# Kernel tuning notes

Measured on AMD Instinct MI355X. Metric: run time of the kernel, lower is better.

The kernel has to match this reference:

```python
import jax, jax.numpy as jnp
import numpy as np

EMBED_DIM = 512
N_HEADS = 8
HEAD_DIM = EMBED_DIM // N_HEADS


def setup_inputs() -> dict:
    key = jax.random.key(0)
    ks = jax.random.split(key, 8)
    B, S, D = 8, 2048, EMBED_DIM
    scale = 1.0 / np.sqrt(D)
    return {
        "key": jax.random.normal(ks[0], (B, S, D), dtype=jnp.float32),
        "query": jax.random.normal(ks[1], (B, S, D), dtype=jnp.float32),
        "value": jax.random.normal(ks[2], (B, S, D), dtype=jnp.float32),
        # nn.Linear stores weight as [out, in]; y = x @ W.T. We store W_T=[in,out].
        "Wq": jax.random.normal(ks[3], (D, D), dtype=jnp.float32) * scale,
        "Wk": jax.random.normal(ks[4], (D, D), dtype=jnp.float32) * scale,
        "Wv": jax.random.normal(ks[5], (D, D), dtype=jnp.float32) * scale,
        "Wo": jax.random.normal(ks[6], (D, D), dtype=jnp.float32) * scale,
        "bo": jax.random.normal(ks[7], (D,), dtype=jnp.float32) * scale,
    }


def reference(key, query, value, Wq, Wk, Wv, Wo, bo):
    B, S, D = key.shape
    Sq = query.shape[1]
    H, Hd = N_HEADS, HEAD_DIM
    # projections (no bias for q/k/v)
    q = (query @ Wq).reshape(B, Sq, H, Hd)
    k = (key @ Wk).reshape(B, S, H, Hd)
    v = (value @ Wv).reshape(B, S, H, Hd)
    # scores: [B, H, Sq, S]
    product = jnp.einsum("bqhd,bkhd->bhqk", q, k) / np.sqrt(Hd)
    scores = jax.nn.softmax(product, axis=-1)
    out = jnp.einsum("bhqk,bkhd->bqhd", scores, v).reshape(B, Sq, D)
    return out @ Wo + bo
```

## Files before the change

kernel.cpp:

```cpp
#include <hip/hip_runtime.h>

typedef _Float16 half8 __attribute__((ext_vector_type(8)));
typedef _Float16 half4 __attribute__((ext_vector_type(4)));
typedef __fp16 fp16x2 __attribute__((ext_vector_type(2)));
typedef float floatx16 __attribute__((ext_vector_type(16)));

#define MFMA_F16 __builtin_amdgcn_mfma_f32_32x32x16_f16

__device__ __forceinline__ float fast_exp2(float x) {
#if __has_builtin(__builtin_amdgcn_exp2f)
    return __builtin_amdgcn_exp2f(x);
#else
    return exp2f(x);
#endif
}

__device__ __forceinline__ half4 pack4(float a, float b, float c, float d) {
    union { fp16x2 p[2]; half4 h; } u;
    u.p[0] = __builtin_amdgcn_cvt_pkrtz(a, b);
    u.p[1] = __builtin_amdgcn_cvt_pkrtz(c, d);
    return u.h;
}

__device__ __forceinline__ half8 ld_frag_lds(const _Float16* p) {
    union { half8 v; half4 h[2]; } u;
    u.h[0] = *(const half4*)(p);
    u.h[1] = *(const half4*)(p + 4);
    return u.v;
}

__global__ __launch_bounds__(256) void wcvt_kernel(const float* __restrict__ Wq,
                                                   const float* __restrict__ Wk,
                                                   const float* __restrict__ Wv,
                                                   const float* __restrict__ Wo,
                                                   _Float16* __restrict__ Wt) {
    __shared__ _Float16 T[64 * 68];
    const int bx   = blockIdx.x;
    const int wsel = bx >> 6;
    const int tile = bx & 63;
    const int to   = (tile >> 3) * 64;
    const int ti   = (tile & 7) * 64;
    const float* src = (wsel == 0) ? Wq : (wsel == 1) ? Wk : (wsel == 2) ? Wv : Wo;
    const int t = threadIdx.x;
    const int rloc = t >> 4, c4 = (t & 15) * 4;
#pragma unroll
    for (int m = 0; m < 4; m++) {
        int i = ti + rloc + 16 * m;
        float4 f = *(const float4*)(src + (size_t)i * 512 + to + c4);
        T[(c4 + 0) * 68 + rloc + 16 * m] = (_Float16)f.x;
        T[(c4 + 1) * 68 + rloc + 16 * m] = (_Float16)f.y;
        T[(c4 + 2) * 68 + rloc + 16 * m] = (_Float16)f.z;
        T[(c4 + 3) * 68 + rloc + 16 * m] = (_Float16)f.w;
    }
    __syncthreads();
    const int o_loc = t >> 2, ich = (t & 3) * 16;
    const _Float16* s = &T[o_loc * 68 + ich];
    _Float16* dst = Wt + (size_t)wsel * 262144 + (size_t)(to + o_loc) * 512 + ti + ich;
    half4 a0 = *(const half4*)(s);
    half4 a1 = *(const half4*)(s + 4);
    half4 a2 = *(const half4*)(s + 8);
    half4 a3 = *(const half4*)(s + 12);
    *(half4*)(dst)      = a0;
    *(half4*)(dst + 4)  = a1;
    *(half4*)(dst + 8)  = a2;
    *(half4*)(dst + 12) = a3;
}

__global__ __launch_bounds__(256, 3) void qkv_gemm(const float* __restrict__ query,
                                                   const float* __restrict__ key,
                                                   const float* __restrict__ value,
                                                   const _Float16* __restrict__ Wt,
                                                   _Float16* __restrict__ Qh,
                                                   _Float16* __restrict__ Kh,
                                                   _Float16* __restrict__ Vt,
                                                   float C1) {
    __shared__ _Float16 Alds[128 * 68];
    __shared__ _Float16 Blds[128 * 68];

    const int z = blockIdx.z;
    const float* A = (z == 0) ? query : (z == 1) ? key : value;
    const _Float16* W = Wt + (size_t)z * 262144;

    const int tid  = threadIdx.x;
    const int lane = tid & 63;
    const int w    = tid >> 6;
    const int l31  = lane & 31;
    const int lh   = lane >> 5;
    const int wm   = w >> 1;
    const int wn   = w & 1;
    const int n0   = blockIdx.x * 128;
    const int m0   = blockIdx.y * 128;
    const int crow = tid >> 3;
    const int ck8  = (tid & 7) * 8;

    floatx16 acc[2][2];
#pragma unroll
    for (int i = 0; i < 2; i++)
#pragma unroll
        for (int j = 0; j < 2; j++)
#pragma unroll
            for (int r = 0; r < 16; r++) acc[i][j][r] = 0.0f;

    float4 apre[4][2];
    int4   bpre[4];
#pragma unroll
    for (int i = 0; i < 4; i++) {
        const float* p = A + (size_t)(m0 + crow + 32 * i) * 512 + ck8;
        apre[i][0] = *(const float4*)(p);
        apre[i][1] = *(const float4*)(p + 4);
        bpre[i] = *(const int4*)(W + (size_t)(n0 + crow + 32 * i) * 512 + ck8);
    }

    for (int t = 0; t < 8; t++) {
        __syncthreads();
#pragma unroll
        for (int i = 0; i < 4; i++) {
            int r = crow + 32 * i;
            float4 f0 = apre[i][0], f1 = apre[i][1];
            *(half4*)&Alds[r * 68 + ck8]     = pack4(f0.x, f0.y, f0.z, f0.w);
            *(half4*)&Alds[r * 68 + ck8 + 4] = pack4(f1.x, f1.y, f1.z, f1.w);
            *(int2*)&Blds[r * 68 + ck8]      = make_int2(bpre[i].x, bpre[i].y);
            *(int2*)&Blds[r * 68 + ck8 + 4]  = make_int2(bpre[i].z, bpre[i].w);
        }
        __syncthreads();
        if (t < 7) {
            int ks2 = (t + 1) * 64;
#pragma unroll
            for (int i = 0; i < 4; i++) {
                const float* p = A + (size_t)(m0 + crow + 32 * i) * 512 + ks2 + ck8;
                apre[i][0] = *(const float4*)(p);
                apre[i][1] = *(const float4*)(p + 4);
                bpre[i] = *(const int4*)(W + (size_t)(n0 + crow + 32 * i) * 512 + ks2 + ck8);
            }
        }
#pragma unroll
        for (int kc = 0; kc < 4; kc++) {
            int kb = kc * 16 + lh * 8;
            half8 af[2], bf[2];
            af[0] = ld_frag_lds(&Alds[(wm * 64 + l31) * 68 + kb]);
            af[1] = ld_frag_lds(&Alds[(wm * 64 + 32 + l31) * 68 + kb]);
            bf[0] = ld_frag_lds(&Blds[(wn * 64 + l31) * 68 + kb]);
            bf[1] = ld_frag_lds(&Blds[(wn * 64 + 32 + l31) * 68 + kb]);
#pragma unroll
            for (int i = 0; i < 2; i++)
#pragma unroll
                for (int j = 0; j < 2; j++)
                    acc[i][j] = MFMA_F16(af[i], bf[j], acc[i][j], 0, 0, 0);
        }
    }

    const float oscale = (z == 0) ? C1 : 1.0f;
    _Float16* out01 = (z == 0) ? Qh : Kh;
#pragma unroll
    for (int i = 0; i < 2; i++) {
#pragma unroll
        for (int j = 0; j < 2; j++) {
            int gn    = n0 + wn * 64 + j * 32 + l31;
            int mbase = m0 + wm * 64 + i * 32 + 4 * lh;
            int h = gn >> 6, hd = gn & 63;
            if (z < 2) {
#pragma unroll
                for (int r = 0; r < 16; r++) {
                    int gm = mbase + (r & 3) + 8 * (r >> 2);
                    int b = gm >> 11, s = gm & 2047;
                    out01[(size_t)((b * 8 + h) * 2048 + s) * 64 + hd] =
                        (_Float16)(acc[i][j][r] * oscale);
                }
            } else {
#pragma unroll
                for (int g = 0; g < 4; g++) {
                    int gm = mbase + 8 * g;
                    int b = gm >> 11, s = gm & 2047;
                    *(half4*)&Vt[(size_t)((b * 8 + h) * 64 + hd) * 2048 + s] =
                        pack4(acc[i][j][4 * g + 0], acc[i][j][4 * g + 1],
                              acc[i][j][4 * g + 2], acc[i][j][4 * g + 3]);
                }
            }
        }
    }
}

__global__ __launch_bounds__(256, 3) void out_gemm(const _Float16* __restrict__ A,
                                                   const _Float16* __restrict__ W,
                                                   const float* __restrict__ bias,
                                                   float* __restrict__ out) {
    __shared__ _Float16 Alds[128 * 68];
    __shared__ _Float16 Blds[128 * 68];

    const int tid  = threadIdx.x;
    const int lane = tid & 63;
    const int w    = tid >> 6;
    const int l31  = lane & 31;
    const int lh   = lane >> 5;
    const int wm   = w >> 1;
    const int wn   = w & 1;
    const int n0   = blockIdx.x * 128;
    const int m0   = blockIdx.y * 128;
    const int crow = tid >> 3;
    const int ck8  = (tid & 7) * 8;

    floatx16 acc[2][2];
#pragma unroll
    for (int i = 0; i < 2; i++)
#pragma unroll
        for (int j = 0; j < 2; j++)
#pragma unroll
            for (int r = 0; r < 16; r++) acc[i][j][r] = 0.0f;

    int4 apre[4], bpre[4];
#pragma unroll
    for (int i = 0; i < 4; i++) {
        apre[i] = *(const int4*)(A + (size_t)(m0 + crow + 32 * i) * 512 + ck8);
        bpre[i] = *(const int4*)(W + (size_t)(n0 + crow + 32 * i) * 512 + ck8);
    }

    for (int t = 0; t < 8; t++) {
        __syncthreads();
#pragma unroll
        for (int i = 0; i < 4; i++) {
            int r = crow + 32 * i;
            *(int2*)&Alds[r * 68 + ck8]     = make_int2(apre[i].x, apre[i].y);
            *(int2*)&Alds[r * 68 + ck8 + 4] = make_int2(apre[i].z, apre[i].w);
            *(int2*)&Blds[r * 68 + ck8]     = make_int2(bpre[i].x, bpre[i].y);
            *(int2*)&Blds[r * 68 + ck8 + 4] = make_int2(bpre[i].z, bpre[i].w);
        }
        __syncthreads();
        if (t < 7) {
            int ks2 = (t + 1) * 64;
#pragma unroll
            for (int i = 0; i < 4; i++) {
                apre[i] = *(const int4*)(A + (size_t)(m0 + crow + 32 * i) * 512 + ks2 + ck8);
                bpre[i] = *(const int4*)(W + (size_t)(n0 + crow + 32 * i) * 512 + ks2 + ck8);
            }
        }
#pragma unroll
        for (int kc = 0; kc < 4; kc++) {
            int kb = kc * 16 + lh * 8;
            half8 af[2], bf[2];
            af[0] = ld_frag_lds(&Alds[(wm * 64 + l31) * 68 + kb]);
            af[1] = ld_frag_lds(&Alds[(wm * 64 + 32 + l31) * 68 + kb]);
            bf[0] = ld_frag_lds(&Blds[(wn * 64 + l31) * 68 + kb]);
            bf[1] = ld_frag_lds(&Blds[(wn * 64 + 32 + l31) * 68 + kb]);
#pragma unroll
            for (int i = 0; i < 2; i++)
#pragma unroll
                for (int j = 0; j < 2; j++)
                    acc[i][j] = MFMA_F16(af[i], bf[j], acc[i][j], 0, 0, 0);
        }
    }

#pragma unroll
    for (int i = 0; i < 2; i++) {
#pragma unroll
        for (int j = 0; j < 2; j++) {
            int gn    = n0 + wn * 64 + j * 32 + l31;
            int mbase = m0 + wm * 64 + i * 32 + 4 * lh;
            float bv = bias[gn];
#pragma unroll
            for (int r = 0; r < 16; r++) {
                int gm = mbase + (r & 3) + 8 * (r >> 2);
                out[(size_t)gm * 512 + gn] = acc[i][j][r] + bv;
            }
        }
    }
}

__global__ __launch_bounds__(256, 4) void attn_kernel(const _Float16* __restrict__ Qg,
                                                      const _Float16* __restrict__ Kg,
                                                      const _Float16* __restrict__ Vg,
                                                      _Float16* __restrict__ AO) {
    __shared__ _Float16 Klds[64 * 68];
    __shared__ _Float16 Vlds[64 * 68];
    __shared__ _Float16 Plds[4][32 * 68];

    const int tid  = threadIdx.x;
    const int lane = tid & 63;
    const int w    = tid >> 6;
    const int l31  = lane & 31;
    const int lh   = lane >> 5;
    const int h    = blockIdx.y;
    const int b    = blockIdx.z;
    const int q0   = blockIdx.x * 128 + w * 32;

    const size_t bhoff = (size_t)(b * 8 + h) * (2048 * 64);
    const _Float16* Qbh = Qg + bhoff;
    const _Float16* Kbh = Kg + bhoff;
    const _Float16* Vbh = Vg + bhoff;

    const int c0row = tid >> 3, ck8 = (tid & 7) * 8;
    const int c1row = c0row + 32;

    half8 qf[4];
#pragma unroll
    for (int kc = 0; kc < 4; kc++)
        qf[kc] = *(const half8*)(Qbh + (size_t)(q0 + l31) * 64 + kc * 16 + lh * 8);

    floatx16 O[2];
#pragma unroll
    for (int i = 0; i < 2; i++)
#pragma unroll
        for (int r = 0; r < 16; r++) O[i][r] = 0.0f;
    float lsum = 0.0f;

    int4 kpre[2], vpre[2];
    kpre[0] = *(const int4*)(Kbh + c0row * 64 + ck8);
    kpre[1] = *(const int4*)(Kbh + c1row * 64 + ck8);
    vpre[0] = *(const int4*)(Vbh + (size_t)c0row * 2048 + ck8);
    vpre[1] = *(const int4*)(Vbh + (size_t)c1row * 2048 + ck8);

    for (int kt = 0; kt < 32; kt++) {
        __syncthreads();
        *(int2*)&Klds[c0row * 68 + ck8]     = make_int2(kpre[0].x, kpre[0].y);
        *(int2*)&Klds[c0row * 68 + ck8 + 4] = make_int2(kpre[0].z, kpre[0].w);
        *(int2*)&Klds[c1row * 68 + ck8]     = make_int2(kpre[1].x, kpre[1].y);
        *(int2*)&Klds[c1row * 68 + ck8 + 4] = make_int2(kpre[1].z, kpre[1].w);
        *(int2*)&Vlds[c0row * 68 + ck8]     = make_int2(vpre[0].x, vpre[0].y);
        *(int2*)&Vlds[c0row * 68 + ck8 + 4] = make_int2(vpre[0].z, vpre[0].w);
        *(int2*)&Vlds[c1row * 68 + ck8]     = make_int2(vpre[1].x, vpre[1].y);
        *(int2*)&Vlds[c1row * 68 + ck8 + 4] = make_int2(vpre[1].z, vpre[1].w);
        __syncthreads();

        if (kt < 31) {
            const _Float16* Ksrc = Kbh + (size_t)(kt + 1) * 4096;
            const _Float16* Vsrc = Vbh + (size_t)(kt + 1) * 64;
            kpre[0] = *(const int4*)(Ksrc + c0row * 64 + ck8);
            kpre[1] = *(const int4*)(Ksrc + c1row * 64 + ck8);
            vpre[0] = *(const int4*)(Vsrc + (size_t)c0row * 2048 + ck8);
            vpre[1] = *(const int4*)(Vsrc + (size_t)c1row * 2048 + ck8);
        }

        floatx16 Sf[2];
#pragma unroll
        for (int i = 0; i < 2; i++)
#pragma unroll
            for (int r = 0; r < 16; r++) Sf[i][r] = 0.0f;
#pragma unroll
        for (int ms = 0; ms < 2; ms++)
#pragma unroll
            for (int kc = 0; kc < 4; kc++) {
                half8 kf = ld_frag_lds(&Klds[(ms * 32 + l31) * 68 + kc * 16 + lh * 8]);
                Sf[ms] = MFMA_F16(kf, qf[kc], Sf[ms], 0, 0, 0);
            }

        float rsA = 0.0f, rsB = 0.0f;
#pragma unroll
        for (int ms = 0; ms < 2; ms++) {
#pragma unroll
            for (int g = 0; g < 4; g++) {
                float p0 = fast_exp2(Sf[ms][4 * g + 0]);
                float p1 = fast_exp2(Sf[ms][4 * g + 1]);
                float p2 = fast_exp2(Sf[ms][4 * g + 2]);
                float p3 = fast_exp2(Sf[ms][4 * g + 3]);
                rsA += p0 + p1;
                rsB += p2 + p3;
                *(half4*)&Plds[w][l31 * 68 + ms * 32 + g * 8 + lh * 4] =
                    pack4(p0, p1, p2, p3);
            }
        }
        lsum += rsA + rsB;

#pragma unroll
        for (int kc = 0; kc < 4; kc++) {
            half8 pf = ld_frag_lds(&Plds[w][l31 * 68 + kc * 16 + lh * 8]);
#pragma unroll
            for (int hs = 0; hs < 2; hs++) {
                half8 vf = ld_frag_lds(&Vlds[(hs * 32 + l31) * 68 + kc * 16 + lh * 8]);
                O[hs] = MFMA_F16(vf, pf, O[hs], 0, 0, 0);
            }
        }
    }

    lsum += __shfl_xor(lsum, 32);
    float inv = 1.0f / lsum;
    int q = q0 + l31;
#pragma unroll
    for (int hs = 0; hs < 2; hs++) {
#pragma unroll
        for (int g = 0; g < 4; g++) {
            *(half4*)&AO[(size_t)(b * 2048 + q) * 512 + h * 64 + hs * 32 + g * 8 + lh * 4] =
                pack4(O[hs][4 * g + 0] * inv, O[hs][4 * g + 1] * inv,
                      O[hs][4 * g + 2] * inv, O[hs][4 * g + 3] * inv);
        }
    }
}

extern "C" void kernel_launch(void* const* d_in, const int* in_sizes, int n_in,
                              void* d_out, int out_size, void* d_ws, size_t ws_size,
                              hipStream_t stream) {
    const float* key   = (const float*)d_in[0];
    const float* query = (const float*)d_in[1];
    const float* value = (const float*)d_in[2];
    const float* Wq    = (const float*)d_in[3];
    const float* Wk    = (const float*)d_in[4];
    const float* Wv    = (const float*)d_in[5];
    const float* Wo    = (const float*)d_in[6];
    const float* bo    = (const float*)d_in[7];

    _Float16* ws = (_Float16*)d_ws;
    _Float16* Wt = ws;
    _Float16* Qh = ws + 1048576;
    _Float16* Kh = Qh + 8388608;
    _Float16* Vt = Kh + 8388608;
    _Float16* AO = Vt + 8388608;

    const float C1 = 0.18033688011112042f;

    wcvt_kernel<<<dim3(256), dim3(256), 0, stream>>>(Wq, Wk, Wv, Wo, Wt);

    qkv_gemm<<<dim3(4, 128, 3), dim3(256), 0, stream>>>(query, key, value, Wt,
                                                        Qh, Kh, Vt, C1);

    attn_kernel<<<dim3(16, 8, 8), dim3(256), 0, stream>>>(Qh, Kh, Vt, AO);

    out_gemm<<<dim3(4, 128), dim3(256), 0, stream>>>(AO, Wt + 3 * 262144, bo,
                                                     (float*)d_out);
}
```

Measured before the change: 298.1 us.

## Double-buffer K/V in LDS and software-pipeline PV matmul one tile behind

The attention kernel now keeps two LDS buffers for K and V tiles, so each iteration needs a single barrier instead of two, and it prefetches two tiles ahead from global memory. The P·V product for the previous tile is deferred into the next iteration, with V fragments held in registers, so the exp/softmax work can overlap with the MFMA work. This costs more registers and LDS, and the occupancy hint drops from 4 to 3 blocks per CU.

```diff
diff --git a/kernel.cpp b/kernel.cpp
--- a/kernel.cpp
+++ b/kernel.cpp
@@ -265,12 +265,12 @@
     }
 }
 
-__global__ __launch_bounds__(256, 4) void attn_kernel(const _Float16* __restrict__ Qg,
+__global__ __launch_bounds__(256, 3) void attn_kernel(const _Float16* __restrict__ Qg,
                                                       const _Float16* __restrict__ Kg,
                                                       const _Float16* __restrict__ Vg,
                                                       _Float16* __restrict__ AO) {
-    __shared__ _Float16 Klds[64 * 68];
-    __shared__ _Float16 Vlds[64 * 68];
+    __shared__ _Float16 Kbuf[2][64 * 68];
+    __shared__ _Float16 Vbuf[2][64 * 68];
     __shared__ _Float16 Plds[4][32 * 68];
 
     const int tid  = threadIdx.x;
@@ -286,6 +286,7 @@
     const _Float16* Qbh = Qg + bhoff;
     const _Float16* Kbh = Kg + bhoff;
     const _Float16* Vbh = Vg + bhoff;
+    _Float16* Pw = Plds[w];
 
     const int c0row = tid >> 3, ck8 = (tid & 7) * 8;
     const int c1row = c0row + 32;
@@ -301,73 +302,116 @@
 #pragma unroll
         for (int r = 0; r < 16; r++) O[i][r] = 0.0f;
     float lsum = 0.0f;
+
+    half4 Ppack[8];
+    half8 vf[4][2];
 
     int4 kpre[2], vpre[2];
     kpre[0] = *(const int4*)(Kbh + c0row * 64 + ck8);
     kpre[1] = *(const int4*)(Kbh + c1row * 64 + ck8);
     vpre[0] = *(const int4*)(Vbh + (size_t)c0row * 2048 + ck8);
     vpre[1] = *(const int4*)(Vbh + (size_t)c1row * 2048 + ck8);
+    *(int2*)&Kbuf[0][c0row * 68 + ck8]     = make_int2(kpre[0].x, kpre[0].y);
+    *(int2*)&Kbuf[0][c0row * 68 + ck8 + 4] = make_int2(kpre[0].z, kpre[0].w);
+    *(int2*)&Kbuf[0][c1row * 68 + ck8]     = make_int2(kpre[1].x, kpre[1].y);
+    *(int2*)&Kbuf[0][c1row * 68 + ck8 + 4] = make_int2(kpre[1].z, kpre[1].w);
+    *(int2*)&Vbuf[0][c0row * 68 + ck8]     = make_int2(vpre[0].x, vpre[0].y);
+    *(int2*)&Vbuf[0][c0row * 68 + ck8 + 4] = make_int2(vpre[0].z, vpre[0].w);
+    *(int2*)&Vbuf[0][c1row * 68 + ck8]     = make_int2(vpre[1].x, vpre[1].y);
+    *(int2*)&Vbuf[0][c1row * 68 + ck8 + 4] = make_int2(vpre[1].z, vpre[1].w);
+    kpre[0] = *(const int4*)(Kbh + 4096 + c0row * 64 + ck8);
+    kpre[1] = *(const int4*)(Kbh + 4096 + c1row * 64 + ck8);
+    vpre[0] = *(const int4*)(Vbh + 64 + (size_t)c0row * 2048 + ck8);
+    vpre[1] = *(const int4*)(Vbh + 64 + (size_t)c1row * 2048 + ck8);
+    __syncthreads();
 
     for (int kt = 0; kt < 32; kt++) {
-        __syncthreads();
-        *(int2*)&Klds[c0row * 68 + ck8]     = make_int2(kpre[0].x, kpre[0].y);
-        *(int2*)&Klds[c0row * 68 + ck8 + 4] = make_int2(kpre[0].z, kpre[0].w);
-        *(int2*)&Klds[c1row * 68 + ck8]     = make_int2(kpre[1].x, kpre[1].y);
-        *(int2*)&Klds[c1row * 68 + ck8 + 4] = make_int2(kpre[1].z, kpre[1].w);
-        *(int2*)&Vlds[c0row * 68 + ck8]     = make_int2(vpre[0].x, vpre[0].y);
-        *(int2*)&Vlds[c0row * 68 + ck8 + 4] = make_int2(vpre[0].z, vpre[0].w);
-        *(int2*)&Vlds[c1row * 68 + ck8]     = make_int2(vpre[1].x, vpre[1].y);
-        *(int2*)&Vlds[c1row * 68 + ck8 + 4] = make_int2(vpre[1].z, vpre[1].w);
-        __syncthreads();
+        const int cur = kt & 1;
+        const _Float16* Kc = Kbuf[cur];
+        const _Float16* Vc = Vbuf[cur];
+
+        if (kt > 0) {
+#pragma unroll
+            for (int i = 0; i < 8; i++) {
+                int ms = i >> 2, g = i & 3;
+                *(half4*)&Pw[l31 * 68 + ms * 32 + g * 8 + lh * 4] = Ppack[i];
+            }
+#pragma unroll
+            for (int kc = 0; kc < 4; kc++) {
+                half8 pf = ld_frag_lds(&Pw[l31 * 68 + kc * 16 + lh * 8]);
+                O[0] = MFMA_F16(vf[kc][0], pf, O[0], 0, 0, 0);
+                O[1] = MFMA_F16(vf[kc][1], pf, O[1], 0, 0, 0);
+            }
+        }
 
         if (kt < 31) {
-            const _Float16* Ksrc = Kbh + (size_t)(kt + 1) * 4096;
-            const _Float16* Vsrc = Vbh + (size_t)(kt + 1) * 64;
+            _Float16* Kd = Kbuf[cur ^ 1];
+            _Float16* Vd = Vbuf[cur ^ 1];
+            *(int2*)&Kd[c0row * 68 + ck8]     = make_int2(kpre[0].x, kpre[0].y);
+            *(int2*)&Kd[c0row * 68 + ck8 + 4] = make_int2(kpre[0].z, kpre[0].w);
+            *(int2*)&Kd[c1row * 68 + ck8]     = make_int2(kpre[1].x, kpre[1].y);
+            *(int2*)&Kd[c1row * 68 + ck8 + 4] = make_int2(kpre[1].z, kpre[1].w);
+            *(int2*)&Vd[c0row * 68 + ck8]     = make_int2(vpre[0].x, vpre[0].y);
+            *(int2*)&Vd[c0row * 68 + ck8 + 4] = make_int2(vpre[0].z, vpre[0].w);
+            *(int2*)&Vd[c1row * 68 + ck8]     = make_int2(vpre[1].x, vpre[1].y);
+            *(int2*)&Vd[c1row * 68 + ck8 + 4] = make_int2(vpre[1].z, vpre[1].w);
+        }
+        if (kt < 30) {
+            const _Float16* Ksrc = Kbh + (size_t)(kt + 2) * 4096;
+            const _Float16* Vsrc = Vbh + (size_t)(kt + 2) * 64;
             kpre[0] = *(const int4*)(Ksrc + c0row * 64 + ck8);
             kpre[1] = *(const int4*)(Ksrc + c1row * 64 + ck8);
             vpre[0] = *(const int4*)(Vsrc + (size_t)c0row * 2048 + ck8);
             vpre[1] = *(const int4*)(Vsrc + (size_t)c1row * 2048 + ck8);
         }
 
+#pragma unroll
+        for (int kc = 0; kc < 4; kc++) {
+            vf[kc][0] = ld_frag_lds(&Vc[(l31)*68      + kc * 16 + lh * 8]);
+            vf[kc][1] = ld_frag_lds(&Vc[(32 + l31)*68 + kc * 16 + lh * 8]);
+        }
+
         floatx16 Sf[2];
 #pragma unroll
         for (int i = 0; i < 2; i++)
 #pragma unroll
             for (int r = 0; r < 16; r++) Sf[i][r] = 0.0f;
 #pragma unroll
-        for (int ms = 0; ms < 2; ms++)
-#pragma unroll
-            for (int kc = 0; kc < 4; kc++) {
-                half8 kf = ld_frag_lds(&Klds[(ms * 32 + l31) * 68 + kc * 16 + lh * 8]);
+        for (int kc = 0; kc < 4; kc++) {
+#pragma unroll
+            for (int ms = 0; ms < 2; ms++) {
+                half8 kf = ld_frag_lds(&Kc[(ms * 32 + l31) * 68 + kc * 16 + lh * 8]);
                 Sf[ms] = MFMA_F16(kf, qf[kc], Sf[ms], 0, 0, 0);
             }
+        }
 
         float rsA = 0.0f, rsB = 0.0f;
 #pragma unroll
-        for (int ms = 0; ms < 2; ms++) {
-#pragma unroll
-            for (int g = 0; g < 4; g++) {
-                float p0 = fast_exp2(Sf[ms][4 * g + 0]);
-                float p1 = fast_exp2(Sf[ms][4 * g + 1]);
-                float p2 = fast_exp2(Sf[ms][4 * g + 2]);
-                float p3 = fast_exp2(Sf[ms][4 * g + 3]);
-                rsA += p0 + p1;
-                rsB += p2 + p3;
-                *(half4*)&Plds[w][l31 * 68 + ms * 32 + g * 8 + lh * 4] =
-                    pack4(p0, p1, p2, p3);
-            }
+        for (int i = 0; i < 8; i++) {
+            int ms = i >> 2, g = i & 3;
+            float p0 = fast_exp2(Sf[ms][4 * g + 0]);
+            float p1 = fast_exp2(Sf[ms][4 * g + 1]);
+            float p2 = fast_exp2(Sf[ms][4 * g + 2]);
+            float p3 = fast_exp2(Sf[ms][4 * g + 3]);
+            rsA += p0 + p1;
+            rsB += p2 + p3;
+            Ppack[i] = pack4(p0, p1, p2, p3);
         }
         lsum += rsA + rsB;
 
-#pragma unroll
-        for (int kc = 0; kc < 4; kc++) {
-            half8 pf = ld_frag_lds(&Plds[w][l31 * 68 + kc * 16 + lh * 8]);
-#pragma unroll
-            for (int hs = 0; hs < 2; hs++) {
-                half8 vf = ld_frag_lds(&Vlds[(hs * 32 + l31) * 68 + kc * 16 + lh * 8]);
-                O[hs] = MFMA_F16(vf, pf, O[hs], 0, 0, 0);
-            }
-        }
+        __syncthreads();
+    }
+
+#pragma unroll
+    for (int i = 0; i < 8; i++) {
+        int ms = i >> 2, g = i & 3;
+        *(half4*)&Pw[l31 * 68 + ms * 32 + g * 8 + lh * 4] = Ppack[i];
+    }
+#pragma unroll
+    for (int kc = 0; kc < 4; kc++) {
+        half8 pf = ld_frag_lds(&Pw[l31 * 68 + kc * 16 + lh * 8]);
+        O[0] = MFMA_F16(vf[kc][0], pf, O[0], 0, 0, 0);
+        O[1] = MFMA_F16(vf[kc][1], pf, O[1], 0, 0, 0);
     }
 
     lsum += __shfl_xor(lsum, 32);
```

After: 297.5 us. About the same (-0.2%).
